# Kernel tuning notes

Measured on AMD Instinct MI355X. Metric: run time of the kernel, lower is better.

The kernel has to match this reference:

```python
import jax, jax.numpy as jnp
import numpy as np

HIDDEN = 896
NUM_Q_HEADS = 14
NUM_KV_HEADS = 2
HEAD_DIM = 64
ROPE_BASE = 10000.0
B, S = 4, 2048


def rotate_half(x):
    x1, x2 = jnp.split(x, 2, axis=-1)
    return jnp.concatenate((-x2, x1), axis=-1)


def rope_cos_sin(position_ids):
    # position_ids: [B, S] int -> cos/sin [B, 1, S, HEAD_DIM]
    inv_freq = 1.0 / (ROPE_BASE ** (jnp.arange(0, HEAD_DIM, 2, dtype=jnp.float32) / HEAD_DIM))
    freqs = position_ids.astype(jnp.float32)[..., None] * inv_freq  # [B,S,D/2]
    emb = jnp.concatenate((freqs, freqs), axis=-1)  # [B,S,D]
    return jnp.cos(emb)[:, None, :, :], jnp.sin(emb)[:, None, :, :]


def setup_inputs() -> dict:
    key = jax.random.key(0)
    k1, k2, k3, k4, k5 = jax.random.split(key, 5)
    s = 1.0 / np.sqrt(HIDDEN)
    return {
        "hidden_states": jax.random.normal(k1, (B, S, HIDDEN), dtype=jnp.float32),
        "position_ids": jnp.broadcast_to(jnp.arange(S, dtype=jnp.int64), (B, S)),
        "Wq": jax.random.normal(k2, (HIDDEN, NUM_Q_HEADS * HEAD_DIM), dtype=jnp.float32) * s,
        "Wk": jax.random.normal(k3, (HIDDEN, NUM_KV_HEADS * HEAD_DIM), dtype=jnp.float32) * s,
        "Wv": jax.random.normal(k4, (HIDDEN, NUM_KV_HEADS * HEAD_DIM), dtype=jnp.float32) * s,
        "Wo": jax.random.normal(k5, (NUM_Q_HEADS * HEAD_DIM, HIDDEN), dtype=jnp.float32) * s,
    }


def reference(hidden_states, position_ids, Wq, Wk, Wv, Wo):
    b, s, _ = hidden_states.shape
    n_rep = NUM_Q_HEADS // NUM_KV_HEADS

    q = (hidden_states @ Wq).reshape(b, s, NUM_Q_HEADS, HEAD_DIM).transpose(0, 2, 1, 3)   # [B,Hq,S,D]
    k = (hidden_states @ Wk).reshape(b, s, NUM_KV_HEADS, HEAD_DIM).transpose(0, 2, 1, 3)  # [B,Hkv,S,D]
    v = (hidden_states @ Wv).reshape(b, s, NUM_KV_HEADS, HEAD_DIM).transpose(0, 2, 1, 3)

    cos, sin = rope_cos_sin(position_ids)  # [B,1,S,D]
    q = q * cos + rotate_half(q) * sin
    k = k * cos + rotate_half(k) * sin

    # repeat_interleave KV heads to match query heads
    k = jnp.repeat(k, n_rep, axis=1)  # [B,Hq,S,D]
    v = jnp.repeat(v, n_rep, axis=1)

    scale = 1.0 / jnp.sqrt(jnp.float32(HEAD_DIM))
    attn = jnp.einsum('bhqd,bhkd->bhqk', q, k) * scale  # [B,Hq,S,S]
    attn = jax.nn.softmax(attn, axis=-1)
    out = jnp.einsum('bhqk,bhkd->bhqd', attn, v)  # [B,Hq,S,D]
    out = out.transpose(0, 2, 1, 3).reshape(b, s, NUM_Q_HEADS * HEAD_DIM)
    return out @ Wo
```

## Files before the change

kernel.cpp:

```cpp
#include <hip/hip_runtime.h>
#include <hip/hip_bf16.h>
#include <math.h>

typedef unsigned short ushort_t;
typedef __bf16 bf16x8 __attribute__((ext_vector_type(8)));
typedef float f32x4 __attribute__((ext_vector_type(4)));

#define HIDDEN 896
#define NQH 14
#define NKVH 2
#define HD 64
#define SEQ 2048
#define NBATCH 4

__device__ inline ushort_t f2bf(float x) {
  union { float f; unsigned u; } c; c.f = x;
  unsigned r = c.u + 0x7FFFu + ((c.u >> 16) & 1u);
  return (ushort_t)(r >> 16);
}

__device__ inline unsigned pack2bf(float a, float b) {
  union { float f; unsigned u; } ca, cb; ca.f = a; cb.f = b;
  unsigned ua = ca.u + 0x8000u, ub = cb.u + 0x8000u;
  return __builtin_amdgcn_perm(ub, ua, 0x07060302);
}

__device__ inline bf16x8 ldfrag(const ushort_t* p) {
  return *reinterpret_cast<const bf16x8*>(p);
}

__device__ inline void async16(const ushort_t* g, ushort_t* l) {
  __builtin_amdgcn_global_load_lds(
      (const __attribute__((address_space(1))) void*)g,
      (__attribute__((address_space(3))) void*)l, 16, 0, 0);
}


__device__ inline void transpose_sec(const float* __restrict__ in, ushort_t* __restrict__ out,
                                     int K, int N, int bx, int by) {
  __shared__ float tile[32][33];
  int k0 = by * 32, n0 = bx * 32;
  for (int r = threadIdx.y; r < 32; r += 8) {
    int k = k0 + r, n = n0 + threadIdx.x;
    tile[r][threadIdx.x] = (k < K && n < N) ? in[(size_t)k * N + n] : 0.f;
  }
  __syncthreads();
  for (int r = threadIdx.y; r < 32; r += 8) {
    int n = n0 + r, k = k0 + threadIdx.x;
    if (n < N && k < K) out[(size_t)n * K + k] = f2bf(tile[threadIdx.x][r]);
  }
}

__global__ void k_prep(const float* __restrict__ hidden, ushort_t* __restrict__ hb,
                       const float* __restrict__ Wq, const float* __restrict__ Wk,
                       const float* __restrict__ Wv, const float* __restrict__ Wo,
                       ushort_t* __restrict__ wT, ushort_t* __restrict__ woT,
                       float2* __restrict__ ctab) {
  const int blk = blockIdx.x;
  const int tid = threadIdx.y * 32 + threadIdx.x;
  if (blk < 7168) {
    int i = blk * 256 + tid;
    float4 v = reinterpret_cast<const float4*>(hidden)[i];
    ushort4 o;
    o.x = f2bf(v.x); o.y = f2bf(v.y); o.z = f2bf(v.z); o.w = f2bf(v.w);
    reinterpret_cast<ushort4*>(hb)[i] = o;
  } else if (blk < 7424) {
    int idx = (blk - 7168) * 256 + tid;
    int s = idx >> 5, dp = idx & 31;
    float inv = exp2f(-(float)dp * 0.41524101186092596f);
    float ang = (float)s * inv;
    float sn, cn;
    sincosf(ang, &sn, &cn);
    ctab[idx] = make_float2(cn, sn);
  } else if (blk < 8208) {
    int t = blk - 7424;
    transpose_sec(Wq, wT, 896, 896, t % 28, t / 28);
  } else if (blk < 8320) {
    int t = blk - 8208;
    transpose_sec(Wk, wT + (size_t)896 * 896, 896, 128, t % 4, t / 4);
  } else if (blk < 8432) {
    int t = blk - 8320;
    transpose_sec(Wv, wT + (size_t)1024 * 896, 896, 128, t % 4, t / 4);
  } else {
    int t = blk - 8432;
    transpose_sec(Wo, woT, 896, 896, t % 28, t / 28);
  }
}

__global__ __launch_bounds__(256) void k_qkv(
    const ushort_t* __restrict__ hb,
    const ushort_t* __restrict__ wT,
    const int* __restrict__ pos_ids,
    const float2* __restrict__ ctab,
    ushort_t* __restrict__ Qg,
    ushort_t* __restrict__ Kg,
    ushort_t* __restrict__ Vtg) {
  __shared__ ushort_t sa[128 * 32];
  __shared__ ushort_t sbb[128 * 32];

  const int sect = blockIdx.x;
  const int nt0 = sect * 128;
  const int m0 = blockIdx.y * 128;
  const int tid = threadIdx.x;
  const int wave = tid >> 6, lane = tid & 63;
  const int l15 = lane & 15, quad = lane >> 4;
  const int wm = wave >> 1, wn = wave & 1;

  f32x4 acc[4][4];
  const f32x4 z4 = {0.f, 0.f, 0.f, 0.f};
#pragma unroll
  for (int a = 0; a < 4; ++a)
#pragma unroll
    for (int b = 0; b < 4; ++b) acc[a][b] = z4;

  for (int kt = 0; kt < 28; ++kt) {
    const int k0 = kt * 32;
    __syncthreads();
#pragma unroll
    for (int i = 0; i < 2; ++i) {
      int c = wave * 128 + i * 64 + lane;
      async16(hb + (size_t)(m0 + (c >> 2)) * HIDDEN + k0 + (c & 3) * 8,
              sa + (size_t)(wave * 128 + i * 64) * 8);
      async16(wT + (size_t)(nt0 + (c >> 2)) * HIDDEN + k0 + (c & 3) * 8,
              sbb + (size_t)(wave * 128 + i * 64) * 8);
    }
    __syncthreads();
    bf16x8 bf[4], af[4];
#pragma unroll
    for (int nb = 0; nb < 4; ++nb)
      bf[nb] = ldfrag(sbb + ((wn * 64 + nb * 16 + l15) * 32 + quad * 8));
#pragma unroll
    for (int mb = 0; mb < 4; ++mb)
      af[mb] = ldfrag(sa + ((wm * 64 + mb * 16 + l15) * 32 + quad * 8));
#pragma unroll
    for (int mb = 0; mb < 4; ++mb)
#pragma unroll
      for (int nb = 0; nb < 4; ++nb)
        acc[mb][nb] = __builtin_amdgcn_mfma_f32_16x16x32_bf16(af[mb], bf[nb], acc[mb][nb], 0, 0, 0);
  }

  if (sect < 8) {
    const bool isQ = sect < 7;
    const float csc = isQ ? 0.125f * 1.4426950408889634f : 1.0f;
    ushort_t* dst = isQ ? Qg : Kg;
    const int nheads = isQ ? NQH : NKVH;
    const int hh = isQ ? sect * 2 + wn : wn;
#pragma unroll
    for (int mb = 0; mb < 4; ++mb)
#pragma unroll
      for (int r = 0; r < 4; ++r) {
        int token = m0 + wm * 64 + mb * 16 + quad * 4 + r;
        int b = token >> 11, s = token & 2047;
        int pos = pos_ids[token];
        size_t base = ((size_t)(b * nheads + hh) * SEQ + s) * HD;
#pragma unroll
        for (int nb = 0; nb < 2; ++nb) {
          float2 cs = ctab[pos * 32 + nb * 16 + l15];
          float x0 = acc[mb][nb][r];
          float x1 = acc[mb][nb + 2][r];
          float y0 = (x0 * cs.x - x1 * cs.y) * csc;
          float y1 = (x1 * cs.x + x0 * cs.y) * csc;
          dst[base + nb * 16 + l15]      = f2bf(y0);
          dst[base + nb * 16 + l15 + 32] = f2bf(y1);
        }
      }
  } else {
#pragma unroll
    for (int mb = 0; mb < 4; ++mb) {
      int token0 = m0 + wm * 64 + mb * 16 + quad * 4;
      int b = token0 >> 11, s = token0 & 2047;
#pragma unroll
      for (int nb = 0; nb < 4; ++nb) {
        int d = nb * 16 + l15;
        uint2 pk;
        pk.x = pack2bf(acc[mb][nb][0], acc[mb][nb][1]);
        pk.y = pack2bf(acc[mb][nb][2], acc[mb][nb][3]);
        *reinterpret_cast<uint2*>(Vtg + ((size_t)(b * NKVH + wn) * HD + d) * SEQ + s) = pk;
      }
    }
  }
}

__global__ __launch_bounds__(256) void k_attn(
    const ushort_t* __restrict__ Qg,
    const ushort_t* __restrict__ Kg,
    const ushort_t* __restrict__ Vtg,
    ushort_t* __restrict__ attn) {
  __shared__ ushort_t kbuf[2][64 * 64];
  __shared__ ushort_t vbuf[2][64 * 64];
  __shared__ ushort_t pbuf[4][32 * 72];

  const int qt = blockIdx.x;
  const int bh = blockIdx.y;
  const int b = bh / NQH, h = bh % NQH;
  const int kvh = h / (NQH / NKVH);
  const int tid = threadIdx.x;
  const int wave = tid >> 6, lane = tid & 63;
  const int l15 = lane & 15, quad = lane >> 4;
  const int q0 = qt * 128;

  bf16x8 qf[2][2];
#pragma unroll
  for (int qs = 0; qs < 2; ++qs) {
    const size_t qb = ((size_t)bh * SEQ + q0 + wave * 32 + qs * 16 + l15) * HD + quad * 8;
    qf[qs][0] = ldfrag(Qg + qb);
    qf[qs][1] = ldfrag(Qg + qb + 32);
  }

  const size_t kbase = (size_t)(b * NKVH + kvh) * SEQ * HD;
  const size_t vbase = (size_t)(b * NKVH + kvh) * HD * SEQ;

  const int srow = tid >> 3;
  const int sc0 = (tid & 7) ^ (srow & 7);
  const int srow2 = (256 + tid) >> 3;
  const int sc2 = (tid & 7) ^ (srow2 & 7);
  const int sbase1 = wave * 64 * 8;
  const int sbase2 = (256 + wave * 64) * 8;

  float l_part[2] = {0.f, 0.f};
  f32x4 o[2][4];
  const f32x4 z4 = {0.f, 0.f, 0.f, 0.f};
#pragma unroll
  for (int qs = 0; qs < 2; ++qs)
#pragma unroll
    for (int nb = 0; nb < 4; ++nb) o[qs][nb] = z4;

  ushort_t* pw = pbuf[wave];

  async16(Kg + kbase + (size_t)srow * HD + sc0 * 8, kbuf[0] + sbase1);
  async16(Vtg + vbase + (size_t)srow * SEQ + sc0 * 8, vbuf[0] + sbase1);
  async16(Kg + kbase + (size_t)srow2 * HD + sc2 * 8, kbuf[0] + sbase2);
  async16(Vtg + vbase + (size_t)srow2 * SEQ + sc2 * 8, vbuf[0] + sbase2);

  for (int jt = 0; jt < 32; ++jt) {
    const int cur = jt & 1;
    __syncthreads();
    if (jt + 1 < 32) {
      const int nxt = cur ^ 1;
      const int s1 = (jt + 1) * 64;
      async16(Kg + kbase + (size_t)(s1 + srow) * HD + sc0 * 8, kbuf[nxt] + sbase1);
      async16(Vtg + vbase + (size_t)srow * SEQ + s1 + sc0 * 8, vbuf[nxt] + sbase1);
      async16(Kg + kbase + (size_t)(s1 + srow2) * HD + sc2 * 8, kbuf[nxt] + sbase2);
      async16(Vtg + vbase + (size_t)srow2 * SEQ + s1 + sc2 * 8, vbuf[nxt] + sbase2);
    }

    const ushort_t* kb = kbuf[cur];
    const ushort_t* vb = vbuf[cur];

#pragma unroll
    for (int nb = 0; nb < 4; ++nb) {
      int row = nb * 16 + l15;
      int sw = row & 7;
      bf16x8 kf0 = ldfrag(kb + (row * 8 + (quad ^ sw)) * 8);
      bf16x8 kf1 = ldfrag(kb + (row * 8 + ((4 + quad) ^ sw)) * 8);
#pragma unroll
      for (int qs = 0; qs < 2; ++qs) {
        f32x4 t = z4;
        t = __builtin_amdgcn_mfma_f32_16x16x32_bf16(kf0, qf[qs][0], t, 0, 0, 0);
        t = __builtin_amdgcn_mfma_f32_16x16x32_bf16(kf1, qf[qs][1], t, 0, 0, 0);
        float p0 = __builtin_amdgcn_exp2f(t[0]);
        float p1 = __builtin_amdgcn_exp2f(t[1]);
        float p2 = __builtin_amdgcn_exp2f(t[2]);
        float p3 = __builtin_amdgcn_exp2f(t[3]);
        l_part[qs] += (p0 + p1) + (p2 + p3);
        uint2 d;
        d.x = pack2bf(p0, p1);
        d.y = pack2bf(p2, p3);
        *reinterpret_cast<uint2*>(pw + (qs * 16 + l15) * 72 + nb * 16 + quad * 4) = d;
      }
    }

    bf16x8 pf[2][2];
#pragma unroll
    for (int qs = 0; qs < 2; ++qs) {
      pf[qs][0] = ldfrag(pw + (qs * 16 + l15) * 72 + quad * 8);
      pf[qs][1] = ldfrag(pw + (qs * 16 + l15) * 72 + 32 + quad * 8);
    }
#pragma unroll
    for (int nb = 0; nb < 4; ++nb) {
      int row = nb * 16 + l15;
      int sw = row & 7;
      bf16x8 vf0 = ldfrag(vb + (row * 8 + (quad ^ sw)) * 8);
      bf16x8 vf1 = ldfrag(vb + (row * 8 + ((4 + quad) ^ sw)) * 8);
#pragma unroll
      for (int qs = 0; qs < 2; ++qs) {
        o[qs][nb] = __builtin_amdgcn_mfma_f32_16x16x32_bf16(pf[qs][0], vf0, o[qs][nb], 0, 0, 0);
        o[qs][nb] = __builtin_amdgcn_mfma_f32_16x16x32_bf16(pf[qs][1], vf1, o[qs][nb], 0, 0, 0);
      }
    }
  }

#pragma unroll
  for (int qs = 0; qs < 2; ++qs) {
    float s = l_part[qs];
    s += __shfl_xor(s, 16);
    s += __shfl_xor(s, 32);
    l_part[qs] = s;
  }

#pragma unroll
  for (int qs = 0; qs < 2; ++qs) {
    float il = 1.0f / l_part[qs];
#pragma unroll
    for (int r = 0; r < 4; ++r) {
      float inv = __shfl(il, quad * 4 + r);
      int qg = q0 + wave * 32 + qs * 16 + quad * 4 + r;
#pragma unroll
      for (int nb = 0; nb < 4; ++nb) {
        float val = o[qs][nb][r] * inv;
        attn[(size_t)(b * SEQ + qg) * (NQH * HD) + h * HD + nb * 16 + l15] = f2bf(val);
      }
    }
  }
}

__global__ __launch_bounds__(256) void k_oproj(
    const ushort_t* __restrict__ attn,
    const ushort_t* __restrict__ woT,
    float* __restrict__ out) {
  __shared__ ushort_t sa[128 * 32];
  __shared__ ushort_t sbb[128 * 32];

  const int n0 = blockIdx.x * 128;
  const int m0 = blockIdx.y * 128;
  const int tid = threadIdx.x;
  const int wave = tid >> 6, lane = tid & 63;
  const int l15 = lane & 15, quad = lane >> 4;
  const int wm = wave >> 1, wn = wave & 1;

  f32x4 acc[4][4];
  const f32x4 z4 = {0.f, 0.f, 0.f, 0.f};
#pragma unroll
  for (int a = 0; a < 4; ++a)
#pragma unroll
    for (int b = 0; b < 4; ++b) acc[a][b] = z4;

  for (int kt = 0; kt < 28; ++kt) {
    const int k0 = kt * 32;
    __syncthreads();
#pragma unroll
    for (int i = 0; i < 2; ++i) {
      int c = wave * 128 + i * 64 + lane;
      async16(attn + (size_t)(m0 + (c >> 2)) * HIDDEN + k0 + (c & 3) * 8,
              sa + (size_t)(wave * 128 + i * 64) * 8);
      async16(woT + (size_t)(n0 + (c >> 2)) * HIDDEN + k0 + (c & 3) * 8,
              sbb + (size_t)(wave * 128 + i * 64) * 8);
    }
    __syncthreads();
    bf16x8 bf[4], af[4];
#pragma unroll
    for (int nb = 0; nb < 4; ++nb)
      bf[nb] = ldfrag(sbb + ((wn * 64 + nb * 16 + l15) * 32 + quad * 8));
#pragma unroll
    for (int mb = 0; mb < 4; ++mb)
      af[mb] = ldfrag(sa + ((wm * 64 + mb * 16 + l15) * 32 + quad * 8));
#pragma unroll
    for (int mb = 0; mb < 4; ++mb)
#pragma unroll
      for (int nb = 0; nb < 4; ++nb)
        acc[mb][nb] = __builtin_amdgcn_mfma_f32_16x16x32_bf16(af[mb], bf[nb], acc[mb][nb], 0, 0, 0);
  }

#pragma unroll
  for (int mb = 0; mb < 4; ++mb)
#pragma unroll
    for (int nb = 0; nb < 4; ++nb)
#pragma unroll
      for (int r = 0; r < 4; ++r)
        out[(size_t)(m0 + wm * 64 + mb * 16 + quad * 4 + r) * HIDDEN +
            n0 + wn * 64 + nb * 16 + l15] = acc[mb][nb][r];
}


extern "C" void kernel_launch(void* const* d_in, const int* in_sizes, int n_in,
                              void* d_out, int out_size, void* d_ws, size_t ws_size,
                              hipStream_t stream) {
  (void)in_sizes; (void)n_in; (void)out_size; (void)ws_size;
  const float* hidden = (const float*)d_in[0];
  const int* pos      = (const int*)d_in[1];
  const float* Wq     = (const float*)d_in[2];
  const float* Wk     = (const float*)d_in[3];
  const float* Wv     = (const float*)d_in[4];
  const float* Wo     = (const float*)d_in[5];
  float* out = (float*)d_out;

  char* ws = (char*)d_ws;
  ushort_t* hb   = (ushort_t*)(ws);
  ushort_t* wT   = (ushort_t*)(ws + 14680064);
  float2*   ctab = (float2*)  (ws + 16744448);
  ushort_t* Qg   = (ushort_t*)(ws + 17268736);
  ushort_t* Kg   = (ushort_t*)(ws + 31948800);
  ushort_t* Vtg  = (ushort_t*)(ws + 34045952);
  ushort_t* attn = (ushort_t*)(ws + 36143104);
  ushort_t* woT  = (ushort_t*)(ws + 50823168);

  k_prep<<<9216, dim3(32, 8), 0, stream>>>(hidden, hb, Wq, Wk, Wv, Wo, wT, woT, ctab);
  k_qkv<<<dim3(9, 64), 256, 0, stream>>>(hb, wT, pos, ctab, Qg, Kg, Vtg);
  k_attn<<<dim3(16, 56), 256, 0, stream>>>(Qg, Kg, Vtg, attn);
  k_oproj<<<dim3(7, 64), 256, 0, stream>>>(attn, woT, out);
}
```

Baseline: 270.3 us.

## Remap block indices for XCD locality, single-buffer KV, compute row sums via MFMA

Flattens the grids of the QKV, attention and output-projection kernels and remaps block IDs so that groups of 8 consecutive blocks (likely spread across the 8 XCDs) share K/V heads or weight sections, aiming for better L2 reuse. The attention kernel drops double-buffered K/V loads in favour of a single buffer with a sync on each side of the load. The softmax denominator is now computed by an MFMA against a ones vector instead of scalar adds plus shuffles. Removing the prefetch exposes global-load latency on every tile, and the row sum now uses bf16-rounded probabilities.

```diff
diff --git a/kernel.cpp b/kernel.cpp
--- a/kernel.cpp
+++ b/kernel.cpp
@@ -98,9 +98,12 @@
   __shared__ ushort_t sa[128 * 32];
   __shared__ ushort_t sbb[128 * 32];
 
-  const int sect = blockIdx.x;
+  const int f = blockIdx.x;
+  const int x = f & 7, s8 = f >> 3;
+  const int sect = s8 % 9;
+  const int mt = (s8 / 9) * 8 + x;
   const int nt0 = sect * 128;
-  const int m0 = blockIdx.y * 128;
+  const int m0 = mt * 128;
   const int tid = threadIdx.x;
   const int wave = tid >> 6, lane = tid & 63;
   const int l15 = lane & 15, quad = lane >> 4;
@@ -186,14 +189,17 @@
     const ushort_t* __restrict__ Kg,
     const ushort_t* __restrict__ Vtg,
     ushort_t* __restrict__ attn) {
-  __shared__ ushort_t kbuf[2][64 * 64];
-  __shared__ ushort_t vbuf[2][64 * 64];
+  __shared__ ushort_t kbuf[64 * 64];
+  __shared__ ushort_t vbuf[64 * 64];
   __shared__ ushort_t pbuf[4][32 * 72];
 
-  const int qt = blockIdx.x;
-  const int bh = blockIdx.y;
-  const int b = bh / NQH, h = bh % NQH;
-  const int kvh = h / (NQH / NKVH);
+  const int f = blockIdx.x;
+  const int x = f & 7, s8 = f >> 3;
+  const int lh = s8 >> 4;
+  const int qt = s8 & 15;
+  const int b = x >> 1, kvh = x & 1;
+  const int h = kvh * 7 + lh;
+  const int bh = b * NQH + h;
   const int tid = threadIdx.x;
   const int wave = tid >> 6, lane = tid & 63;
   const int l15 = lane & 15, quad = lane >> 4;
@@ -206,6 +212,10 @@
     qf[qs][0] = ldfrag(Qg + qb);
     qf[qs][1] = ldfrag(Qg + qb + 32);
   }
+
+  bf16x8 ones;
+#pragma unroll
+  for (int i = 0; i < 8; ++i) ones[i] = (__bf16)1.0f;
 
   const size_t kbase = (size_t)(b * NKVH + kvh) * SEQ * HD;
   const size_t vbase = (size_t)(b * NKVH + kvh) * HD * SEQ;
@@ -217,42 +227,33 @@
   const int sbase1 = wave * 64 * 8;
   const int sbase2 = (256 + wave * 64) * 8;
 
-  float l_part[2] = {0.f, 0.f};
   f32x4 o[2][4];
+  f32x4 lfr[2];
   const f32x4 z4 = {0.f, 0.f, 0.f, 0.f};
 #pragma unroll
-  for (int qs = 0; qs < 2; ++qs)
+  for (int qs = 0; qs < 2; ++qs) {
+    lfr[qs] = z4;
 #pragma unroll
     for (int nb = 0; nb < 4; ++nb) o[qs][nb] = z4;
+  }
 
   ushort_t* pw = pbuf[wave];
 
-  async16(Kg + kbase + (size_t)srow * HD + sc0 * 8, kbuf[0] + sbase1);
-  async16(Vtg + vbase + (size_t)srow * SEQ + sc0 * 8, vbuf[0] + sbase1);
-  async16(Kg + kbase + (size_t)srow2 * HD + sc2 * 8, kbuf[0] + sbase2);
-  async16(Vtg + vbase + (size_t)srow2 * SEQ + sc2 * 8, vbuf[0] + sbase2);
-
   for (int jt = 0; jt < 32; ++jt) {
-    const int cur = jt & 1;
-    __syncthreads();
-    if (jt + 1 < 32) {
-      const int nxt = cur ^ 1;
-      const int s1 = (jt + 1) * 64;
-      async16(Kg + kbase + (size_t)(s1 + srow) * HD + sc0 * 8, kbuf[nxt] + sbase1);
-      async16(Vtg + vbase + (size_t)srow * SEQ + s1 + sc0 * 8, vbuf[nxt] + sbase1);
-      async16(Kg + kbase + (size_t)(s1 + srow2) * HD + sc2 * 8, kbuf[nxt] + sbase2);
-      async16(Vtg + vbase + (size_t)srow2 * SEQ + s1 + sc2 * 8, vbuf[nxt] + sbase2);
-    }
-
-    const ushort_t* kb = kbuf[cur];
-    const ushort_t* vb = vbuf[cur];
+    const int s0 = jt * 64;
+    __syncthreads();
+    async16(Kg + kbase + (size_t)(s0 + srow) * HD + sc0 * 8, kbuf + sbase1);
+    async16(Vtg + vbase + (size_t)srow * SEQ + s0 + sc0 * 8, vbuf + sbase1);
+    async16(Kg + kbase + (size_t)(s0 + srow2) * HD + sc2 * 8, kbuf + sbase2);
+    async16(Vtg + vbase + (size_t)srow2 * SEQ + s0 + sc2 * 8, vbuf + sbase2);
+    __syncthreads();
 
 #pragma unroll
     for (int nb = 0; nb < 4; ++nb) {
       int row = nb * 16 + l15;
       int sw = row & 7;
-      bf16x8 kf0 = ldfrag(kb + (row * 8 + (quad ^ sw)) * 8);
-      bf16x8 kf1 = ldfrag(kb + (row * 8 + ((4 + quad) ^ sw)) * 8);
+      bf16x8 kf0 = ldfrag(kbuf + (row * 8 + (quad ^ sw)) * 8);
+      bf16x8 kf1 = ldfrag(kbuf + (row * 8 + ((4 + quad) ^ sw)) * 8);
 #pragma unroll
       for (int qs = 0; qs < 2; ++qs) {
         f32x4 t = z4;
@@ -262,7 +263,6 @@
         float p1 = __builtin_amdgcn_exp2f(t[1]);
         float p2 = __builtin_amdgcn_exp2f(t[2]);
         float p3 = __builtin_amdgcn_exp2f(t[3]);
-        l_part[qs] += (p0 + p1) + (p2 + p3);
         uint2 d;
         d.x = pack2bf(p0, p1);
         d.y = pack2bf(p2, p3);
@@ -277,11 +277,16 @@
       pf[qs][1] = ldfrag(pw + (qs * 16 + l15) * 72 + 32 + quad * 8);
     }
 #pragma unroll
+    for (int qs = 0; qs < 2; ++qs) {
+      lfr[qs] = __builtin_amdgcn_mfma_f32_16x16x32_bf16(pf[qs][0], ones, lfr[qs], 0, 0, 0);
+      lfr[qs] = __builtin_amdgcn_mfma_f32_16x16x32_bf16(pf[qs][1], ones, lfr[qs], 0, 0, 0);
+    }
+#pragma unroll
     for (int nb = 0; nb < 4; ++nb) {
       int row = nb * 16 + l15;
       int sw = row & 7;
-      bf16x8 vf0 = ldfrag(vb + (row * 8 + (quad ^ sw)) * 8);
-      bf16x8 vf1 = ldfrag(vb + (row * 8 + ((4 + quad) ^ sw)) * 8);
+      bf16x8 vf0 = ldfrag(vbuf + (row * 8 + (quad ^ sw)) * 8);
+      bf16x8 vf1 = ldfrag(vbuf + (row * 8 + ((4 + quad) ^ sw)) * 8);
 #pragma unroll
       for (int qs = 0; qs < 2; ++qs) {
         o[qs][nb] = __builtin_amdgcn_mfma_f32_16x16x32_bf16(pf[qs][0], vf0, o[qs][nb], 0, 0, 0);
@@ -292,18 +297,9 @@
 
 #pragma unroll
   for (int qs = 0; qs < 2; ++qs) {
-    float s = l_part[qs];
-    s += __shfl_xor(s, 16);
-    s += __shfl_xor(s, 32);
-    l_part[qs] = s;
-  }
-
-#pragma unroll
-  for (int qs = 0; qs < 2; ++qs) {
-    float il = 1.0f / l_part[qs];
 #pragma unroll
     for (int r = 0; r < 4; ++r) {
-      float inv = __shfl(il, quad * 4 + r);
+      float inv = 1.0f / lfr[qs][r];
       int qg = q0 + wave * 32 + qs * 16 + quad * 4 + r;
 #pragma unroll
       for (int nb = 0; nb < 4; ++nb) {
@@ -321,8 +317,12 @@
   __shared__ ushort_t sa[128 * 32];
   __shared__ ushort_t sbb[128 * 32];
 
-  const int n0 = blockIdx.x * 128;
-  const int m0 = blockIdx.y * 128;
+  const int f = blockIdx.x;
+  const int x = f & 7, s8 = f >> 3;
+  const int n_sect = s8 % 7;
+  const int mt = (s8 / 7) * 8 + x;
+  const int n0 = n_sect * 128;
+  const int m0 = mt * 128;
   const int tid = threadIdx.x;
   const int wave = tid >> 6, lane = tid & 63;
   const int l15 = lane & 15, quad = lane >> 4;
@@ -395,7 +395,7 @@
   ushort_t* woT  = (ushort_t*)(ws + 50823168);
 
   k_prep<<<9216, dim3(32, 8), 0, stream>>>(hidden, hb, Wq, Wk, Wv, Wo, wT, woT, ctab);
-  k_qkv<<<dim3(9, 64), 256, 0, stream>>>(hb, wT, pos, ctab, Qg, Kg, Vtg);
-  k_attn<<<dim3(16, 56), 256, 0, stream>>>(Qg, Kg, Vtg, attn);
-  k_oproj<<<dim3(7, 64), 256, 0, stream>>>(attn, woT, out);
-}
+  k_qkv<<<576, 256, 0, stream>>>(hb, wT, pos, ctab, Qg, Kg, Vtg);
+  k_attn<<<896, 256, 0, stream>>>(Qg, Kg, Vtg, attn);
+  k_oproj<<<448, 256, 0, stream>>>(attn, woT, out);
+}
```

New measurement: 255.4 us. 5.5% less time.
